# Optimization experiments

Hardware: AMD Instinct MI355X
Metric: run time of the kernel (lower is better)

## Reference

```python
import jax, jax.numpy as jnp
import numpy as np

DIM = 320
NUM_HEADS = 5
HEAD_DIM = DIM // NUM_HEADS  # 64
SCALE = HEAD_DIM ** -0.5


def setup_inputs() -> dict:
    key = jax.random.key(0)
    k1, k2, k3, k4 = jax.random.split(key, 4)
    B, N, C = 8, 2048, DIM
    x = jax.random.normal(k1, (B, N, C), dtype=jnp.float32)
    # nn.Linear(dim, dim*3, bias=False): weight [3*dim, dim]
    w_qkv = jax.random.normal(k2, (3 * C, C), dtype=jnp.float32) * (C ** -0.5)
    # nn.Linear(dim, dim): weight [dim, dim], bias [dim]
    w_proj = jax.random.normal(k3, (C, C), dtype=jnp.float32) * (C ** -0.5)
    b_proj = jax.random.normal(k4, (C,), dtype=jnp.float32) * 0.01
    return {"x": x, "w_qkv": w_qkv, "w_proj": w_proj, "b_proj": b_proj}


def reference(x, w_qkv, w_proj, b_proj):
    B, N, C = x.shape
    H, D = NUM_HEADS, HEAD_DIM
    # qkv projection: [B, N, 3C] -> [3, B, H, N, D]
    qkv = jnp.einsum('bnc,kc->bnk', x, w_qkv)
    qkv = qkv.reshape(B, N, 3, H, D).transpose(2, 0, 3, 1, 4)
    q, k, v = qkv[0], qkv[1], qkv[2]
    # full attention matrix [B, H, N, N] (retained by original module)
    attn = jnp.einsum('bhnd,bhmd->bhnm', q, k) * SCALE
    attn = jax.nn.softmax(attn, axis=-1)
    # attn_drop p=0 -> identity (eval/deterministic)
    out = jnp.einsum('bhnm,bhmd->bhnd', attn, v)
    out = out.transpose(0, 2, 1, 3).reshape(B, N, C)
    out = jnp.einsum('bnc,oc->bno', out, w_proj) + b_proj
    # proj_drop p=0 -> identity
    return out
```

## Files before the change

### kernel.cpp

```cpp
#include <hip/hip_runtime.h>
#include <hip/hip_bf16.h>


typedef __attribute__((ext_vector_type(8))) short bf16x8;
typedef __attribute__((ext_vector_type(4))) float f32x4;

#define MFMA(a, b, c) __builtin_amdgcn_mfma_f32_16x16x32_bf16((a), (b), (c), 0, 0, 0)

#define QSCALE 0.18033688322643216f

static __device__ inline bf16x8 ld8(const __hip_bfloat16* p) {
    return *reinterpret_cast<const bf16x8*>(p);
}

static __device__ inline unsigned short bfbits(float v) {
    unsigned int u = __builtin_bit_cast(unsigned int, v);
    u += 0x7FFFu + ((u >> 16) & 1u);
    return (unsigned short)(u >> 16);
}

static __device__ inline unsigned int cvtpk(float lo, float hi) {
    unsigned int r;
    asm("v_cvt_pk_bf16_f32 %0, %1, %2" : "=v"(r) : "v"(lo), "v"(hi));
    return r;
}

static __device__ inline void gload_lds16(const __hip_bfloat16* g, __hip_bfloat16* l) {
    __builtin_amdgcn_global_load_lds(
        (const __attribute__((address_space(1))) void*)g,
        (__attribute__((address_space(3))) void*)l, 16, 0, 0);
}

__global__ __launch_bounds__(256)
void cvt_all(const float* __restrict__ x,
             const float* __restrict__ wq,
             const float* __restrict__ wp,
             __hip_bfloat16* __restrict__ xb,
             __hip_bfloat16* __restrict__ wqb,
             __hip_bfloat16* __restrict__ wpb)
{
    const size_t tid = (size_t)blockIdx.x * blockDim.x + threadIdx.x;
    const size_t stride = (size_t)gridDim.x * blockDim.x;
    for (size_t i = tid; i < 1413120u; i += stride) {
        const float4* src; ushort4* dst; size_t j;
        if (i < 1310720u) {
            src = (const float4*)x;  dst = (ushort4*)xb;  j = i;
        } else if (i < 1387520u) {
            src = (const float4*)wq; dst = (ushort4*)wqb; j = i - 1310720u;
        } else {
            src = (const float4*)wp; dst = (ushort4*)wpb; j = i - 1387520u;
        }
        float4 v = src[j];
        ushort4 u;
        u.x = bfbits(v.x); u.y = bfbits(v.y);
        u.z = bfbits(v.z); u.w = bfbits(v.w);
        dst[j] = u;
    }
}

__global__ __launch_bounds__(256)
void qkv_kernel(const __hip_bfloat16* __restrict__ xb,
                const __hip_bfloat16* __restrict__ wqb,
                __hip_bfloat16* __restrict__ qout,
                __hip_bfloat16* __restrict__ kp,
                __hip_bfloat16* __restrict__ vp)
{
    __shared__ __align__(16) __hip_bfloat16 As[2 * 8192];
    __shared__ __align__(16) __hip_bfloat16 Bs[2 * 4096];

    const int tid  = threadIdx.x;
    const int wv   = tid >> 6;
    const int lane = tid & 63;
    const int quad = lane >> 4;
    const int col  = lane & 15;

    const int id  = blockIdx.x;
    const int xcd = id & 7;
    const int r9  = id >> 3;
    const int m0  = (xcd * 16 + r9 / 15) * 128;
    const int ny  = r9 % 15;
    const int n0  = ny * 64;

    auto stage = [&](int k0, int c) {
#pragma unroll
        for (int i = 0; i < 4; ++i) {
            int ch = tid + i * 256;
            int r = ch >> 3, sg = ch & 7;
            gload_lds16(&xb[(size_t)(m0 + r) * 320 + k0 + ((sg ^ (r & 7)) * 8)],
                        &As[c * 8192 + (i * 256 + wv * 64) * 8]);
        }
#pragma unroll
        for (int i = 0; i < 2; ++i) {
            int ch = tid + i * 256;
            int r = ch >> 3, sg = ch & 7;
            gload_lds16(&wqb[(size_t)(n0 + r) * 320 + k0 + ((sg ^ (r & 7)) * 8)],
                        &Bs[c * 4096 + (i * 256 + wv * 64) * 8]);
        }
    };

    f32x4 acc[2][4];
#pragma unroll
    for (int i = 0; i < 2; ++i)
#pragma unroll
        for (int j = 0; j < 4; ++j) acc[i][j] = (f32x4){0.f, 0.f, 0.f, 0.f};

    stage(0, 0);

    for (int kt = 0; kt < 5; ++kt) {
        const int c = kt & 1;
        asm volatile("s_waitcnt vmcnt(0)" ::: "memory");
        __builtin_amdgcn_s_barrier();
        if (kt < 4) stage((kt + 1) * 64, c ^ 1);

        const __hip_bfloat16* Ab = &As[c * 8192];
        const __hip_bfloat16* Bb = &Bs[c * 4096];
#pragma unroll
        for (int hf = 0; hf < 2; ++hf) {
            const int sw = ((hf * 4 + quad) ^ (col & 7)) * 8;
            bf16x8 a0 = ld8(&Ab[(wv * 32 + col) * 64 + sw]);
            bf16x8 a1 = ld8(&Ab[(wv * 32 + 16 + col) * 64 + sw]);
#pragma unroll
            for (int nt = 0; nt < 4; ++nt) {
                bf16x8 b = ld8(&Bb[(nt * 16 + col) * 64 + sw]);
                acc[0][nt] = MFMA(a0, b, acc[0][nt]);
                acc[1][nt] = MFMA(a1, b, acc[1][nt]);
            }
        }
        __builtin_amdgcn_s_barrier();
    }

    const int s = ny / 5;
    const int h = ny % 5;
    unsigned short* qo = (unsigned short*)qout;
    unsigned short* ko = (unsigned short*)kp;
    unsigned short* vo = (unsigned short*)vp;
#pragma unroll
    for (int mt = 0; mt < 2; ++mt) {
#pragma unroll
        for (int nt = 0; nt < 4; ++nt) {
#pragma unroll
            for (int r = 0; r < 4; ++r) {
                int m = m0 + wv * 32 + mt * 16 + quad * 4 + r;
                int d = nt * 16 + col;
                int b = m >> 11, n = m & 2047;
                int bh = b * 5 + h;
                float val = acc[mt][nt][r];
                if (s == 0) {
                    qo[((size_t)bh * 2048 + n) * 64 + d] = bfbits(val * QSCALE);
                } else if (s == 1) {
                    int p = n >> 6, nn = n & 63;
                    size_t a = ((size_t)(bh * 32 + p) * 8 + (d >> 5) * 4 + (nn >> 4)) * 512
                             + (((d >> 3) & 3) * 16 + (nn & 15)) * 8 + (d & 7);
                    ko[a] = bfbits(val);
                } else {
                    int p = n >> 6;
                    size_t a = ((size_t)(bh * 32 + p) * 8 + ((n >> 5) & 1) * 4 + (d >> 4)) * 512
                             + (((n >> 3) & 3) * 16 + (d & 15)) * 8 + (n & 7);
                    vo[a] = bfbits(val);
                }
            }
        }
    }
}

__global__ __launch_bounds__(256)
void attn_kernel(const __hip_bfloat16* __restrict__ Q,
                 const __hip_bfloat16* __restrict__ Kp,
                 const __hip_bfloat16* __restrict__ Vp,
                 __hip_bfloat16* __restrict__ A2)
{
    __shared__ __align__(16) __hip_bfloat16 KV[16384];
    __shared__ __align__(16) unsigned char psraw[18432];

    const int tid  = threadIdx.x;
    const int wv   = tid >> 6;
    const int lane = tid & 63;
    const int quad = lane >> 4;
    const int col  = lane & 15;

    const int id  = blockIdx.x;
    const int xcd = id & 7;
    const int j   = id >> 3;
    const int bh  = xcd * 5 + (j >> 4);
    const int q0w = (j & 15) * 128 + wv * 32;
    const int b   = bh / 5, h = bh % 5;

    char* psb = (char*)psraw + wv * 4608;
    char* ps_w = psb + col * 144 + quad * 8;
    const __hip_bfloat16* ps_r =
        (const __hip_bfloat16*)psb + col * 72 + quad * 8;

    const __hip_bfloat16* kg = Kp + (size_t)bh * 131072;
    const __hip_bfloat16* vg = Vp + (size_t)bh * 131072;
    const __hip_bfloat16* Qh = Q + (size_t)bh * 131072;

    bf16x8 qf[2][2];
#pragma unroll
    for (int mt = 0; mt < 2; ++mt)
#pragma unroll
        for (int hf = 0; hf < 2; ++hf)
            qf[mt][hf] = ld8(&Qh[(q0w + mt * 16 + col) * 64 + hf * 32 + quad * 8]);

    f32x4 lp[2];
    f32x4 o[2][4];
#pragma unroll
    for (int mt = 0; mt < 2; ++mt) {
        lp[mt] = (f32x4){0.f, 0.f, 0.f, 0.f};
#pragma unroll
        for (int dt = 0; dt < 4; ++dt) o[mt][dt] = (f32x4){0.f, 0.f, 0.f, 0.f};
    }

    auto stage = [&](int t, int c) {
        const __hip_bfloat16* kp_ = kg + (size_t)t * 4096 + wv * 1024 + lane * 8;
        const __hip_bfloat16* vp_ = vg + (size_t)t * 4096 + wv * 1024 + lane * 8;
        __hip_bfloat16* kl = &KV[c * 4096 + wv * 1024];
        __hip_bfloat16* vl = &KV[8192 + c * 4096 + wv * 1024];
        gload_lds16(kp_, kl);
        gload_lds16(kp_ + 512, kl + 512);
        gload_lds16(vp_, vl);
        gload_lds16(vp_ + 512, vl + 512);
    };

    stage(0, 0);

    for (int t = 0; t < 32; ++t) {
        const int c = t & 1;
        asm volatile("s_waitcnt vmcnt(0)" ::: "memory");
        __builtin_amdgcn_s_barrier();
        stage((t < 31) ? t + 1 : 31, c ^ 1);

        const __hip_bfloat16* kb = &KV[c * 4096];
        const __hip_bfloat16* vb = &KV[8192 + c * 4096];

        f32x4 s[2][4];
#pragma unroll
        for (int nt = 0; nt < 4; ++nt) {
            bf16x8 k0 = ld8(kb + nt * 512 + lane * 8);
            bf16x8 k1 = ld8(kb + (4 + nt) * 512 + lane * 8);
#pragma unroll
            for (int mt = 0; mt < 2; ++mt) {
                f32x4 z = (f32x4){0.f, 0.f, 0.f, 0.f};
                z = MFMA(k0, qf[mt][0], z);
                z = MFMA(k1, qf[mt][1], z);
                s[mt][nt] = z;
            }
        }

#pragma unroll
        for (int mt = 0; mt < 2; ++mt)
#pragma unroll
            for (int nt = 0; nt < 4; ++nt) {
                f32x4 pv;
#pragma unroll
                for (int r = 0; r < 4; ++r)
                    pv[r] = __builtin_amdgcn_exp2f(s[mt][nt][r]);
                lp[mt] += pv;
                uint2 wpk;
                wpk.x = cvtpk(pv[0], pv[1]);
                wpk.y = cvtpk(pv[2], pv[3]);
                *reinterpret_cast<uint2*>(ps_w + mt * 2304 + nt * 32) = wpk;
            }
        __asm__ volatile("s_waitcnt lgkmcnt(0)" ::: "memory");

#pragma unroll
        for (int mt = 0; mt < 2; ++mt)
#pragma unroll
            for (int kk = 0; kk < 2; ++kk) {
                bf16x8 pf = ld8(ps_r + mt * 1152 + kk * 32);
#pragma unroll
                for (int dt = 0; dt < 4; ++dt) {
                    bf16x8 va = ld8(vb + (kk * 4 + dt) * 512 + lane * 8);
                    o[mt][dt] = MFMA(pf, va, o[mt][dt]);
                }
            }
    }

    float lsum[2];
#pragma unroll
    for (int mt = 0; mt < 2; ++mt) {
        float v = lp[mt][0] + lp[mt][1] + lp[mt][2] + lp[mt][3];
        v += __shfl_xor(v, 16, 64);
        v += __shfl_xor(v, 32, 64);
        lsum[mt] = v;
    }

    float* lw = (float*)psb;
    if (quad == 0) {
#pragma unroll
        for (int mt = 0; mt < 2; ++mt)
            lw[mt * 16 + col] = lsum[mt];
    }
    __asm__ volatile("s_waitcnt lgkmcnt(0)" ::: "memory");

    unsigned short* a2o = (unsigned short*)A2;
#pragma unroll
    for (int mt = 0; mt < 2; ++mt) {
#pragma unroll
        for (int r = 0; r < 4; ++r) {
            int row = mt * 16 + quad * 4 + r;
            float inv = 1.0f / lw[row];
            int grow = q0w + row;
#pragma unroll
            for (int dt = 0; dt < 4; ++dt) {
                int d = dt * 16 + col;
                a2o[((size_t)(b * 2048 + grow)) * 320 + h * 64 + d] =
                    bfbits(o[mt][dt][r] * inv);
            }
        }
    }
}

__global__ __launch_bounds__(256)
void proj_kernel(const __hip_bfloat16* __restrict__ a2,
                 const __hip_bfloat16* __restrict__ wpb,
                 const float* __restrict__ bias,
                 float* __restrict__ out)
{
    __shared__ __align__(16) __hip_bfloat16 As[2 * 8192];
    __shared__ __align__(16) __hip_bfloat16 Bs[2 * 4096];

    const int tid  = threadIdx.x;
    const int wv   = tid >> 6;
    const int lane = tid & 63;
    const int quad = lane >> 4;
    const int col  = lane & 15;

    const int id  = blockIdx.x;
    const int xcd = id & 7;
    const int r9  = id >> 3;
    const int m0  = (xcd * 16 + r9 / 5) * 128;
    const int n0  = (r9 % 5) * 64;

    auto stage = [&](int k0, int c) {
#pragma unroll
        for (int i = 0; i < 4; ++i) {
            int ch = tid + i * 256;
            int r = ch >> 3, sg = ch & 7;
            gload_lds16(&a2[(size_t)(m0 + r) * 320 + k0 + ((sg ^ (r & 7)) * 8)],
                        &As[c * 8192 + (i * 256 + wv * 64) * 8]);
        }
#pragma unroll
        for (int i = 0; i < 2; ++i) {
            int ch = tid + i * 256;
            int r = ch >> 3, sg = ch & 7;
            gload_lds16(&wpb[(size_t)(n0 + r) * 320 + k0 + ((sg ^ (r & 7)) * 8)],
                        &Bs[c * 4096 + (i * 256 + wv * 64) * 8]);
        }
    };

    f32x4 acc[2][4];
#pragma unroll
    for (int i = 0; i < 2; ++i)
#pragma unroll
        for (int j = 0; j < 4; ++j) acc[i][j] = (f32x4){0.f, 0.f, 0.f, 0.f};

    stage(0, 0);

    for (int kt = 0; kt < 5; ++kt) {
        const int c = kt & 1;
        asm volatile("s_waitcnt vmcnt(0)" ::: "memory");
        __builtin_amdgcn_s_barrier();
        if (kt < 4) stage((kt + 1) * 64, c ^ 1);

        const __hip_bfloat16* Ab = &As[c * 8192];
        const __hip_bfloat16* Bb = &Bs[c * 4096];
#pragma unroll
        for (int hf = 0; hf < 2; ++hf) {
            const int sw = ((hf * 4 + quad) ^ (col & 7)) * 8;
            bf16x8 a0 = ld8(&Ab[(wv * 32 + col) * 64 + sw]);
            bf16x8 a1 = ld8(&Ab[(wv * 32 + 16 + col) * 64 + sw]);
#pragma unroll
            for (int nt = 0; nt < 4; ++nt) {
                bf16x8 b = ld8(&Bb[(nt * 16 + col) * 64 + sw]);
                acc[0][nt] = MFMA(a0, b, acc[0][nt]);
                acc[1][nt] = MFMA(a1, b, acc[1][nt]);
            }
        }
        __builtin_amdgcn_s_barrier();
    }

#pragma unroll
    for (int nt = 0; nt < 4; ++nt) {
        float bv = bias[n0 + nt * 16 + col];
#pragma unroll
        for (int mt = 0; mt < 2; ++mt) {
#pragma unroll
            for (int r = 0; r < 4; ++r) {
                int m = m0 + wv * 32 + mt * 16 + quad * 4 + r;
                out[(size_t)m * 320 + n0 + nt * 16 + col] = acc[mt][nt][r] + bv;
            }
        }
    }
}

extern "C" void kernel_launch(void* const* d_in, const int* in_sizes, int n_in,
                              void* d_out, int out_size, void* d_ws, size_t ws_size,
                              hipStream_t stream)
{
    const float* x      = (const float*)d_in[0];
    const float* w_qkv  = (const float*)d_in[1];
    const float* w_proj = (const float*)d_in[2];
    const float* b_proj = (const float*)d_in[3];
    float* out = (float*)d_out;

    const size_t NX = 5242880;
    __hip_bfloat16* xb  = (__hip_bfloat16*)d_ws;
    __hip_bfloat16* q   = xb + NX;
    __hip_bfloat16* kp  = q + NX;
    __hip_bfloat16* vp  = kp + NX;
    __hip_bfloat16* wqb = vp + NX;
    __hip_bfloat16* wpb = wqb + 307200;
    __hip_bfloat16* a2  = xb;

    cvt_all<<<1024, 256, 0, stream>>>(x, w_qkv, w_proj, xb, wqb, wpb);
    qkv_kernel<<<1920, 256, 0, stream>>>(xb, wqb, q, kp, vp);
    attn_kernel<<<640, 256, 0, stream>>>(q, kp, vp, a2);
    proj_kernel<<<640, 256, 0, stream>>>(a2, wpb, b_proj, out);
}
```

Measured before the change: 173.2 us.

## Permute K layout so softmax probabilities feed PV MFMA from registers

The K tile layout written by the QKV kernel is permuted so that the QK^T MFMA output lanes already hold the right elements for the A operand of the PV MFMA. Exponentiated scores are packed to bf16 in registers instead of being staged through a shared-memory P buffer, which removes an LDS write, an LDS read and a wait in every iteration. The attention kernel also moves from 256-thread to 128-thread blocks with twice as many blocks, reworks K/V staging across two waves, and drops the P buffer to cut LDS use. In exchange, each block reuses its staged K/V tiles across fewer query rows, so more global and LDS staging traffic is spent per unit of output.

```diff
diff --git a/kernel.cpp b/kernel.cpp
--- a/kernel.cpp
+++ b/kernel.cpp
@@ -4,6 +4,7 @@
 
 typedef __attribute__((ext_vector_type(8))) short bf16x8;
 typedef __attribute__((ext_vector_type(4))) float f32x4;
+typedef __attribute__((ext_vector_type(4))) unsigned int u32x4;
 
 #define MFMA(a, b, c) __builtin_amdgcn_mfma_f32_16x16x32_bf16((a), (b), (c), 0, 0, 0)
 
@@ -149,8 +150,10 @@
                     qo[((size_t)bh * 2048 + n) * 64 + d] = bfbits(val * QSCALE);
                 } else if (s == 1) {
                     int p = n >> 6, nn = n & 63;
-                    size_t a = ((size_t)(bh * 32 + p) * 8 + (d >> 5) * 4 + (nn >> 4)) * 512
-                             + (((d >> 3) & 3) * 16 + (nn & 15)) * 8 + (d & 7);
+                    int ntp = ((nn >> 2) & 1) * 2 + (nn >> 5);
+                    int r16 = ((nn >> 3) & 3) * 4 + (nn & 3);
+                    size_t a = ((size_t)(bh * 32 + p) * 8 + (d >> 5) * 4 + ntp) * 512
+                             + (((d >> 3) & 3) * 16 + r16) * 8 + (d & 7);
                     ko[a] = bfbits(val);
                 } else {
                     int p = n >> 6;
@@ -163,14 +166,13 @@
     }
 }
 
-__global__ __launch_bounds__(256)
+__global__ __launch_bounds__(128)
 void attn_kernel(const __hip_bfloat16* __restrict__ Q,
                  const __hip_bfloat16* __restrict__ Kp,
                  const __hip_bfloat16* __restrict__ Vp,
                  __hip_bfloat16* __restrict__ A2)
 {
     __shared__ __align__(16) __hip_bfloat16 KV[16384];
-    __shared__ __align__(16) unsigned char psraw[18432];
 
     const int tid  = threadIdx.x;
     const int wv   = tid >> 6;
@@ -181,19 +183,29 @@
     const int id  = blockIdx.x;
     const int xcd = id & 7;
     const int j   = id >> 3;
-    const int bh  = xcd * 5 + (j >> 4);
-    const int q0w = (j & 15) * 128 + wv * 32;
+    const int bh  = xcd * 5 + (j >> 5);
+    const int q0w = (j & 31) * 64 + wv * 32;
     const int b   = bh / 5, h = bh % 5;
-
-    char* psb = (char*)psraw + wv * 4608;
-    char* ps_w = psb + col * 144 + quad * 8;
-    const __hip_bfloat16* ps_r =
-        (const __hip_bfloat16*)psb + col * 72 + quad * 8;
 
     const __hip_bfloat16* kg = Kp + (size_t)bh * 131072;
     const __hip_bfloat16* vg = Vp + (size_t)bh * 131072;
     const __hip_bfloat16* Qh = Q + (size_t)bh * 131072;
 
+    auto stage = [&](int t, int c) {
+        const __hip_bfloat16* kp_ = kg + (size_t)t * 4096;
+        const __hip_bfloat16* vp_ = vg + (size_t)t * 4096;
+#pragma unroll
+        for (int i = 0; i < 4; ++i) {
+            int chunk = i * 128 + wv * 64;
+            gload_lds16(kp_ + (size_t)(chunk + lane) * 8,
+                        &KV[c * 4096 + chunk * 8]);
+            gload_lds16(vp_ + (size_t)(chunk + lane) * 8,
+                        &KV[8192 + c * 4096 + chunk * 8]);
+        }
+    };
+
+    stage(0, 0);
+
     bf16x8 qf[2][2];
 #pragma unroll
     for (int mt = 0; mt < 2; ++mt)
@@ -209,25 +221,12 @@
 #pragma unroll
         for (int dt = 0; dt < 4; ++dt) o[mt][dt] = (f32x4){0.f, 0.f, 0.f, 0.f};
     }
-
-    auto stage = [&](int t, int c) {
-        const __hip_bfloat16* kp_ = kg + (size_t)t * 4096 + wv * 1024 + lane * 8;
-        const __hip_bfloat16* vp_ = vg + (size_t)t * 4096 + wv * 1024 + lane * 8;
-        __hip_bfloat16* kl = &KV[c * 4096 + wv * 1024];
-        __hip_bfloat16* vl = &KV[8192 + c * 4096 + wv * 1024];
-        gload_lds16(kp_, kl);
-        gload_lds16(kp_ + 512, kl + 512);
-        gload_lds16(vp_, vl);
-        gload_lds16(vp_ + 512, vl + 512);
-    };
-
-    stage(0, 0);
 
     for (int t = 0; t < 32; ++t) {
         const int c = t & 1;
         asm volatile("s_waitcnt vmcnt(0)" ::: "memory");
         __builtin_amdgcn_s_barrier();
-        stage((t < 31) ? t + 1 : 31, c ^ 1);
+        if (t < 31) stage(t + 1, c ^ 1);
 
         const __hip_bfloat16* kb = &KV[c * 4096];
         const __hip_bfloat16* vb = &KV[8192 + c * 4096];
@@ -246,32 +245,36 @@
             }
         }
 
-#pragma unroll
-        for (int mt = 0; mt < 2; ++mt)
+        bf16x8 pa[2][2];
+#pragma unroll
+        for (int mt = 0; mt < 2; ++mt) {
+            f32x4 pe[4];
 #pragma unroll
             for (int nt = 0; nt < 4; ++nt) {
-                f32x4 pv;
 #pragma unroll
                 for (int r = 0; r < 4; ++r)
-                    pv[r] = __builtin_amdgcn_exp2f(s[mt][nt][r]);
-                lp[mt] += pv;
-                uint2 wpk;
-                wpk.x = cvtpk(pv[0], pv[1]);
-                wpk.y = cvtpk(pv[2], pv[3]);
-                *reinterpret_cast<uint2*>(ps_w + mt * 2304 + nt * 32) = wpk;
-            }
-        __asm__ volatile("s_waitcnt lgkmcnt(0)" ::: "memory");
-
-#pragma unroll
-        for (int mt = 0; mt < 2; ++mt)
+                    pe[nt][r] = __builtin_amdgcn_exp2f(s[mt][nt][r]);
+                lp[mt] += pe[nt];
+            }
 #pragma unroll
             for (int kk = 0; kk < 2; ++kk) {
-                bf16x8 pf = ld8(ps_r + mt * 1152 + kk * 32);
-#pragma unroll
-                for (int dt = 0; dt < 4; ++dt) {
-                    bf16x8 va = ld8(vb + (kk * 4 + dt) * 512 + lane * 8);
-                    o[mt][dt] = MFMA(pf, va, o[mt][dt]);
-                }
+                u32x4 u;
+                u[0] = cvtpk(pe[kk][0], pe[kk][1]);
+                u[1] = cvtpk(pe[kk][2], pe[kk][3]);
+                u[2] = cvtpk(pe[kk + 2][0], pe[kk + 2][1]);
+                u[3] = cvtpk(pe[kk + 2][2], pe[kk + 2][3]);
+                pa[mt][kk] = __builtin_bit_cast(bf16x8, u);
+            }
+        }
+
+#pragma unroll
+        for (int kk = 0; kk < 2; ++kk)
+#pragma unroll
+            for (int dt = 0; dt < 4; ++dt) {
+                bf16x8 va = ld8(vb + (kk * 4 + dt) * 512 + lane * 8);
+#pragma unroll
+                for (int mt = 0; mt < 2; ++mt)
+                    o[mt][dt] = MFMA(pa[mt][kk], va, o[mt][dt]);
             }
     }
 
@@ -284,7 +287,7 @@
         lsum[mt] = v;
     }
 
-    float* lw = (float*)psb;
+    float* lw = (float*)KV + wv * 32;
     if (quad == 0) {
 #pragma unroll
         for (int mt = 0; mt < 2; ++mt)
@@ -414,6 +417,6 @@
 
     cvt_all<<<1024, 256, 0, stream>>>(x, w_qkv, w_proj, xb, wqb, wpb);
     qkv_kernel<<<1920, 256, 0, stream>>>(xb, wqb, q, kp, vp);
-    attn_kernel<<<640, 256, 0, stream>>>(q, kp, vp, a2);
+    attn_kernel<<<1280, 128, 0, stream>>>(q, kp, vp, a2);
     proj_kernel<<<640, 256, 0, stream>>>(a2, wpb, b_proj, out);
 }
```

Result: slower. 189.9 us (+9.6%).
